# Kernel tuning notes

Hardware: AMD Instinct MI355X
Metric: run time of the kernel (lower is better)

## Reference

```python
import jax, jax.numpy as jnp
import numpy as np

B, C_LOCAL, C_GUIDE, C2, H, W = 16, 256, 256, 256, 64, 64
MID = C2 // 2          # mlp hidden channels
CQ = C_LOCAL // 4      # offset_gen hidden channels (also = groups)
EPS = 1e-5             # BatchNorm eps (inference mode)


def _conv(x, w, pad=0, groups=1, b=None):
    out = jax.lax.conv_general_dilated(
        x, w, window_strides=(1, 1), padding=((pad, pad), (pad, pad)),
        dimension_numbers=('NCHW', 'OIHW', 'NCHW'), feature_group_count=groups)
    if b is not None:
        out = out + b[None, :, None, None]
    return out


def _bn(x, g, b, m, v):
    scale = g / jnp.sqrt(v + EPS)
    return x * scale[None, :, None, None] + (b - m * scale)[None, :, None, None]


def _grid_sample(img, grid):
    # img: [C,H,W]; grid: [H,W,2] with (x,y) in [-1,1]; bilinear, zeros padding,
    # align_corners=False (pixel = ((g+1)*size - 1)/2)
    C, Hh, Ww = img.shape
    ix = (grid[..., 0] + 1.0) * (Ww * 0.5) - 0.5
    iy = (grid[..., 1] + 1.0) * (Hh * 0.5) - 0.5
    x0 = jnp.floor(ix); y0 = jnp.floor(iy)
    x1 = x0 + 1.0;      y1 = y0 + 1.0
    wx1 = ix - x0; wx0 = 1.0 - wx1
    wy1 = iy - y0; wy0 = 1.0 - wy1

    def gather(xi, yi):
        valid = (xi >= 0) & (xi < Ww) & (yi >= 0) & (yi < Hh)
        xc = jnp.clip(xi, 0, Ww - 1).astype(jnp.int32)
        yc = jnp.clip(yi, 0, Hh - 1).astype(jnp.int32)
        return img[:, yc, xc] * valid.astype(img.dtype)[None]  # [C,H,W]

    return (gather(x0, y0) * (wx0 * wy0)[None]
            + gather(x1, y0) * (wx1 * wy0)[None]
            + gather(x0, y1) * (wx0 * wy1)[None]
            + gather(x1, y1) * (wx1 * wy1)[None])


def setup_inputs() -> dict:
    key = jax.random.key(0)
    ks = jax.random.split(key, 20)
    w = lambda k, s: jax.random.normal(k, s, jnp.float32) * 0.05
    return {
        'x_local': jax.random.normal(ks[0], (B, C_LOCAL, H, W), jnp.float32),
        'x_guide': jax.random.normal(ks[1], (B, C_GUIDE, H, W), jnp.float32),
        'w_align': w(ks[2], (C2, C_GUIDE, 1, 1)),
        'bn1_g': 1.0 + 0.1 * jax.random.normal(ks[3], (C2,), jnp.float32),
        'bn1_b': 0.1 * jax.random.normal(ks[4], (C2,), jnp.float32),
        'bn1_m': 0.1 * jax.random.normal(ks[5], (C2,), jnp.float32),
        'bn1_v': 0.5 + jax.random.uniform(ks[6], (C2,), jnp.float32),
        'w_off1': w(ks[7], (CQ, 4, 3, 3)),   # grouped: in-ch per group = C_LOCAL/CQ = 4
        'w_off2': w(ks[8], (2, CQ, 1, 1)),
        'b_off2': 0.1 * jax.random.normal(ks[9], (2,), jnp.float32),
        'w_mlp1': w(ks[10], (MID, C_LOCAL, 1, 1)),
        'bn2_g': 1.0 + 0.1 * jax.random.normal(ks[11], (MID,), jnp.float32),
        'bn2_b': 0.1 * jax.random.normal(ks[12], (MID,), jnp.float32),
        'bn2_m': 0.1 * jax.random.normal(ks[13], (MID,), jnp.float32),
        'bn2_v': 0.5 + jax.random.uniform(ks[14], (MID,), jnp.float32),
        'w_mlp2': w(ks[15], (C2, MID, 1, 1)),
    }


def reference(x_local, x_guide, w_align, bn1_g, bn1_b, bn1_m, bn1_v,
              w_off1, w_off2, b_off2, w_mlp1, bn2_g, bn2_b, bn2_m, bn2_v,
              w_mlp2):
    # align(x_guide): 1x1 conv + BN
    g = _bn(_conv(x_guide, w_align), bn1_g, bn1_b, bn1_m, bn1_v)
    # offset_gen(x_local): grouped 3x3 conv -> SiLU -> 1x1 conv (bias) -> [B,2,H,W]
    off = _conv(x_local, w_off1, pad=1, groups=CQ)
    off = _conv(jax.nn.silu(off), w_off2, b=b_off2)
    # base grid in [-1,1], (x,y) last
    ys = jnp.linspace(-1.0, 1.0, H)
    xs = jnp.linspace(-1.0, 1.0, W)
    gy, gx = jnp.meshgrid(ys, xs, indexing='ij')
    base = jnp.stack((gx, gy), axis=-1)                      # [H,W,2]
    v_grid = base[None] + off.transpose(0, 2, 3, 1) * (2.0 / max(H, W))
    g_aligned = jax.vmap(_grid_sample)(g, v_grid)            # [B,C2,H,W]
    # mlp(x_local): 1x1 conv -> BN -> GELU(exact) -> 1x1 conv
    l = _conv(x_local, w_mlp1)
    l = jax.nn.gelu(_bn(l, bn2_g, bn2_b, bn2_m, bn2_v), approximate=False)
    l = _conv(l, w_mlp2)
    return jax.nn.silu(g_aligned + l)
```

## Files before the change

kernel.cpp:

```cpp
#include <hip/hip_runtime.h>

typedef unsigned short u16;
typedef unsigned int u32;
typedef __bf16 bf16x8 __attribute__((ext_vector_type(8)));
typedef float f32x4 __attribute__((ext_vector_type(4)));
typedef u16 u16x4 __attribute__((ext_vector_type(4)));
typedef u16 u16x8 __attribute__((ext_vector_type(8)));

#define EPS 1e-5f

__device__ __forceinline__ u16 f2bf(float f) {
  unsigned u = __builtin_bit_cast(unsigned, f);
  u += 0x7FFFu + ((u >> 16) & 1u);
  return (u16)(u >> 16);
}
__device__ __forceinline__ float bf2f(u16 h) {
  unsigned u = ((unsigned)h) << 16;
  return __builtin_bit_cast(float, u);
}

__global__ void prep_weights(
    const float* __restrict__ wa, const float* __restrict__ g1, const float* __restrict__ b1,
    const float* __restrict__ m1, const float* __restrict__ v1,
    const float* __restrict__ w1, const float* __restrict__ g2, const float* __restrict__ b2,
    const float* __restrict__ m2, const float* __restrict__ v2,
    const float* __restrict__ w2,
    u16* __restrict__ Acat, u16* __restrict__ w1_o,
    float* __restrict__ bias1, float* __restrict__ bias2) {
  int c = blockIdx.x, k = threadIdx.x;
  float s1 = g1[c] / sqrtf(v1[c] + EPS);
  if (k < 256) Acat[c * 384 + k] = f2bf(wa[c * 256 + k] * s1);
  else         Acat[c * 384 + k] = f2bf(w2[c * 128 + (k - 256)]);
  if (c < 128) {
    float s2 = g2[c] / sqrtf(v2[c] + EPS);
    if (k < 256) w1_o[c * 256 + k] = f2bf(w1[c * 256 + k] * s2);
    if (k == 256) bias2[c] = b2[c] - m2[c] * s2;
  }
  if (k == 0) bias1[c] = b1[c] - m1[c] * s1;
}

__global__ __launch_bounds__(256) void gconv_kernel(
    const float* __restrict__ xl, const float* __restrict__ w1,
    u16* __restrict__ sbuf) {
  __shared__ float tile[4][18][68];
  const int tid = threadIdx.x;
  const int band = blockIdx.x;
  const int q = blockIdx.y;
  const int b = blockIdx.z;
  const float* xb = xl + ((size_t)b * 256 + 4 * q) * 4096;

  if (tid < 72) {
    int ci0 = tid / 18, r0_ = tid - ci0 * 18;
    float* rowp = &tile[ci0][r0_][0];
    rowp[0] = 0.f; rowp[65] = 0.f; rowp[66] = 0.f; rowp[67] = 0.f;
  }

  const int ci = tid >> 6, col = tid & 63;
  const int gy0 = band * 16 - 1;
  const float* cp = xb + (size_t)ci * 4096 + col;
  float v[18];
#pragma unroll
  for (int r = 0; r < 18; ++r) {
    int gy = gy0 + r;
    int gyc = min(max(gy, 0), 63);
    float raw = cp[gyc * 64];
    v[r] = ((unsigned)gy < 64u) ? raw : 0.f;
  }
#pragma unroll
  for (int r = 0; r < 18; ++r) tile[ci][r][col + 1] = v[r];

  float wq[36];
#pragma unroll
  for (int i = 0; i < 36; ++i) wq[i] = w1[q * 36 + i];
  __syncthreads();

  const int qx = tid & 15, ry = tid >> 4;
  float a0 = 0.f, a1 = 0.f, a2 = 0.f, a3 = 0.f;
#pragma unroll
  for (int ci2 = 0; ci2 < 4; ++ci2) {
#pragma unroll
    for (int dy = 0; dy < 3; ++dy) {
      const float* rowp = &tile[ci2][ry + dy][qx * 4];
      f32x4 m = *(const f32x4*)rowp;
      float2 e = *(const float2*)(rowp + 4);
      float w0 = wq[ci2 * 9 + dy * 3 + 0];
      float w1_ = wq[ci2 * 9 + dy * 3 + 1];
      float w2_ = wq[ci2 * 9 + dy * 3 + 2];
      a0 += w0 * m[0] + w1_ * m[1] + w2_ * m[2];
      a1 += w0 * m[1] + w1_ * m[2] + w2_ * m[3];
      a2 += w0 * m[2] + w1_ * m[3] + w2_ * e.x;
      a3 += w0 * m[3] + w1_ * e.x  + w2_ * e.y;
    }
  }
  u16x4 o;
  o[0] = f2bf(a0 / (1.f + __expf(-a0)));
  o[1] = f2bf(a1 / (1.f + __expf(-a1)));
  o[2] = f2bf(a2 / (1.f + __expf(-a2)));
  o[3] = f2bf(a3 / (1.f + __expf(-a3)));
  u16* sp = sbuf + ((size_t)(b * 64 + q)) * 4096 + (band * 16 + ry) * 64 + qx * 4;
  *(u16x4*)sp = o;
}

__global__ __launch_bounds__(256) void coords_kernel(
    const u16* __restrict__ sbuf, const float* __restrict__ w2,
    const float* __restrict__ b2, float* __restrict__ coords,
    float* __restrict__ wsum) {
  __shared__ float sw2[128];
  const int tid = threadIdx.x;
  if (tid < 128) sw2[tid] = w2[tid];
  __syncthreads();
  const int b = blockIdx.y;
  const int p = blockIdx.x * 256 + tid;
  const u16* sp = sbuf + (size_t)b * 64 * 4096 + p;
  float ax = 0.f, ay = 0.f;
#pragma unroll 8
  for (int q = 0; q < 64; ++q) {
    float v = bf2f(sp[(size_t)q * 4096]);
    ax += sw2[q] * v;
    ay += sw2[64 + q] * v;
  }
  int y = p >> 6, x = p & 63;
  float ix = (64.f / 63.f) * (float)x + ax + b2[0] - 0.5f;
  float iy = (64.f / 63.f) * (float)y + ay + b2[1] - 0.5f;
  ((float2*)coords)[(size_t)b * 4096 + p] = make_float2(ix, iy);
  float x0f = floorf(ix), y0f = floorf(iy);
  int x0 = (int)x0f, y0 = (int)y0f;
  float wx1 = ix - x0f, wx0 = 1.f - wx1;
  float wy1 = iy - y0f, wy0 = 1.f - wy1;
  bool vx0 = (unsigned)x0 < 64u, vx1 = (unsigned)(x0 + 1) < 64u;
  bool vy0 = (unsigned)y0 < 64u, vy1 = (unsigned)(y0 + 1) < 64u;
  float s = (vx0 && vy0 ? wx0 * wy0 : 0.f) + (vx1 && vy0 ? wx1 * wy0 : 0.f) +
            (vx0 && vy1 ? wx0 * wy1 : 0.f) + (vx1 && vy1 ? wx1 * wy1 : 0.f);
  wsum[(size_t)b * 4096 + p] = s;
}

__global__ __launch_bounds__(256, 1) void sampler_kernel(
    const float* __restrict__ xg, const float* __restrict__ coords,
    u16* __restrict__ xh) {
  __shared__ u16 t[64 * 72];
  const int wg = blockIdx.x;
  const int id = (wg & 7) * 512 + (wg >> 3);
  const int kq = id >> 10;
  const int b = (id >> 6) & 15, row = id & 63;
  const int tid = threadIdx.x;
  const int px = tid & 63, ko = tid >> 6;
  const int p = row * 64 + px;
  float2 cd = ((const float2*)coords)[(size_t)b * 4096 + p];
  float ix = cd.x, iy = cd.y;
  float x0f = floorf(ix), y0f = floorf(iy);
  int x0 = (int)x0f, y0 = (int)y0f;
  float wx1 = ix - x0f, wx0 = 1.f - wx1;
  float wy1 = iy - y0f, wy0 = 1.f - wy1;
  bool vx0 = (unsigned)x0 < 64u, vx1 = (unsigned)(x0 + 1) < 64u;
  bool vy0 = (unsigned)y0 < 64u, vy1 = (unsigned)(y0 + 1) < 64u;
  int x0c = min(max(x0, 0), 63), x1c = min(max(x0 + 1, 0), 63);
  int y0c = min(max(y0, 0), 63), y1c = min(max(y0 + 1, 0), 63);
  float w00 = (vx0 && vy0) ? wx0 * wy0 : 0.f;
  float w10 = (vx1 && vy0) ? wx1 * wy0 : 0.f;
  float w01 = (vx0 && vy1) ? wx0 * wy1 : 0.f;
  float w11 = (vx1 && vy1) ? wx1 * wy1 : 0.f;
  const int i00 = y0c * 64 + x0c, i10 = y0c * 64 + x1c;
  const int i01 = y1c * 64 + x0c, i11 = y1c * 64 + x1c;
  const float* bb = xg + ((size_t)b * 256 + kq * 64 + ko * 16) * 4096;

  float v00[16], v10[16], v01[16], v11[16];
#pragma unroll
  for (int kk = 0; kk < 16; ++kk) {
    const float* bp = bb + (size_t)kk * 4096;
    v00[kk] = bp[i00];
    v10[kk] = bp[i10];
    v01[kk] = bp[i01];
    v11[kk] = bp[i11];
  }
  u16 o[16];
#pragma unroll
  for (int kk = 0; kk < 16; ++kk) {
    float v = w00 * v00[kk] + w10 * v10[kk] + w01 * v01[kk] + w11 * v11[kk];
    o[kk] = f2bf(v);
  }
  *(u16x8*)&t[px * 72 + ko * 16] = *(u16x8*)&o[0];
  *(u16x8*)&t[px * 72 + ko * 16 + 8] = *(u16x8*)&o[8];
  __syncthreads();
  const int seg = tid & 7, pxa = tid >> 3;
  u16* base = xh + ((size_t)b * 4096 + row * 64) * 384 + kq * 64 + seg * 8;
#pragma unroll
  for (int h = 0; h < 2; ++h) {
    int pp = pxa + h * 32;
    *(u16x8*)(base + (size_t)pp * 384) = *(const u16x8*)&t[pp * 72 + seg * 8];
  }
}

__global__ __launch_bounds__(256, 2) void gemm_h(
    const u16* __restrict__ A, const float* __restrict__ Bsrc,
    u16* __restrict__ xh, const float* __restrict__ bias) {
  __shared__ u16 Al[128][40];
  __shared__ u16 Bl[128][40];
  const int tid = threadIdx.x;
  const int b = blockIdx.y;
  const int n0 = blockIdx.x * 128;
  const int wave = tid >> 6, lane = tid & 63;
  const int wr = wave >> 1, wc = wave & 1;
  const int lr = lane & 15, kg = lane >> 4;
  f32x4 acc[4][4] = {};
  const float* Bf = Bsrc + (size_t)b * 256 * 4096;

  for (int kt = 0; kt < 8; ++kt) {
    {
      int m = tid >> 1, pos = (tid & 1) * 16;
      u16x8 v0 = *(const u16x8*)(A + (size_t)m * 256 + kt * 32 + pos);
      u16x8 v1 = *(const u16x8*)(A + (size_t)m * 256 + kt * 32 + pos + 8);
      *(u16x8*)&Al[m][pos] = v0;
      *(u16x8*)&Al[m][pos + 8] = v1;
    }
    {
      int nq = tid & 31, kq = tid >> 5;
      int kb = kt * 32 + kq * 4;
      int nb = n0 + nq * 4;
      f32x4 r[4];
#pragma unroll
      for (int i = 0; i < 4; ++i)
        r[i] = *(const f32x4*)(Bf + (size_t)(kb + i) * 4096 + nb);
#pragma unroll
      for (int j = 0; j < 4; ++j) {
        u16x4 w = {f2bf(r[0][j]), f2bf(r[1][j]), f2bf(r[2][j]), f2bf(r[3][j])};
        *(u16x4*)&Bl[nq * 4 + j][kq * 4] = w;
      }
    }
    __syncthreads();
    bf16x8 af[4], bfr[4];
#pragma unroll
    for (int i = 0; i < 4; ++i) {
      af[i] = *(const bf16x8*)&Al[wr * 64 + i * 16 + lr][kg * 8];
      bfr[i] = *(const bf16x8*)&Bl[wc * 64 + i * 16 + lr][kg * 8];
    }
#pragma unroll
    for (int i = 0; i < 4; ++i)
#pragma unroll
      for (int j = 0; j < 4; ++j)
        acc[i][j] = __builtin_amdgcn_mfma_f32_16x16x32_bf16(af[i], bfr[j], acc[i][j], 0, 0, 0);
    __syncthreads();
  }
  u16* O = xh + (size_t)b * 4096 * 384 + 256;
#pragma unroll
  for (int i = 0; i < 4; ++i) {
    int rb = wr * 64 + i * 16 + kg * 4;
    f32x4 b4 = *(const f32x4*)(bias + rb);
#pragma unroll
    for (int j = 0; j < 4; ++j) {
      int col = n0 + wc * 64 + j * 16 + lr;
      u16x4 w;
#pragma unroll
      for (int e = 0; e < 4; ++e) {
        float v = acc[i][j][e] + b4[e];
        v = 0.5f * v * (1.f + erff(v * 0.70710678118f));
        w[e] = f2bf(v);
      }
      *(u16x4*)(O + (size_t)col * 384 + rb) = w;
    }
  }
}

__global__ __launch_bounds__(256) void gemm_final(
    const u16* __restrict__ A,
    const u16* __restrict__ xh,
    const float* __restrict__ bias1, const float* __restrict__ wsum,
    float* __restrict__ out) {
  __shared__ u16 Al[128][40];
  __shared__ u16 Bl[128][40];
  const int tid = threadIdx.x;
  const int wg = blockIdx.y * 64 + blockIdx.x;
  const int nmb = (wg & 7) * 128 + (wg >> 3);
  const int m = nmb & 1;
  const int n0 = ((nmb >> 1) & 31) * 128;
  const int b = nmb >> 6;
  const int wave = tid >> 6, lane = tid & 63;
  const int wr = wave >> 1, wc = wave & 1;
  const int lr = lane & 15, kg = lane >> 4;
  f32x4 acc[4][4] = {};
  const u16* Ab = A + (size_t)m * 128 * 384;
  const u16* Bb = xh + ((size_t)b * 4096 + n0) * 384;

  for (int kt = 0; kt < 12; ++kt) {
#pragma unroll
    for (int c = 0; c < 2; ++c) {
      int ch = tid + c * 256;
      int r = ch >> 2, pos = (ch & 3) * 8;
      *(u16x8*)&Al[r][pos] = *(const u16x8*)(Ab + (size_t)r * 384 + kt * 32 + pos);
      *(u16x8*)&Bl[r][pos] = *(const u16x8*)(Bb + (size_t)r * 384 + kt * 32 + pos);
    }
    __syncthreads();
    bf16x8 af[4], bfr[4];
#pragma unroll
    for (int i = 0; i < 4; ++i) {
      af[i] = *(const bf16x8*)&Al[wr * 64 + i * 16 + lr][kg * 8];
      bfr[i] = *(const bf16x8*)&Bl[wc * 64 + i * 16 + lr][kg * 8];
    }
#pragma unroll
    for (int i = 0; i < 4; ++i)
#pragma unroll
      for (int j = 0; j < 4; ++j)
        acc[i][j] = __builtin_amdgcn_mfma_f32_16x16x32_bf16(af[i], bfr[j], acc[i][j], 0, 0, 0);
    __syncthreads();
  }

  float* Ob = out + (size_t)b * 256 * 4096;
#pragma unroll
  for (int j = 0; j < 4; ++j) {
    int col = n0 + wc * 64 + j * 16 + lr;
    float ws = wsum[(size_t)b * 4096 + col];
#pragma unroll
    for (int i = 0; i < 4; ++i) {
      int rb = m * 128 + wr * 64 + i * 16 + kg * 4;
      f32x4 b4 = *(const f32x4*)(bias1 + rb);
#pragma unroll
      for (int e = 0; e < 4; ++e) {
        float v = acc[i][j][e] + b4[e] * ws;
        Ob[(size_t)(rb + e) * 4096 + col] = v / (1.f + __expf(-v));
      }
    }
  }
}

extern "C" void kernel_launch(void* const* d_in, const int* in_sizes, int n_in,
                              void* d_out, int out_size, void* d_ws, size_t ws_size,
                              hipStream_t stream) {
  const float* x_local = (const float*)d_in[0];
  const float* x_guide = (const float*)d_in[1];
  const float* w_align = (const float*)d_in[2];
  const float* bn1_g = (const float*)d_in[3];
  const float* bn1_b = (const float*)d_in[4];
  const float* bn1_m = (const float*)d_in[5];
  const float* bn1_v = (const float*)d_in[6];
  const float* w_off1 = (const float*)d_in[7];
  const float* w_off2 = (const float*)d_in[8];
  const float* b_off2 = (const float*)d_in[9];
  const float* w_mlp1 = (const float*)d_in[10];
  const float* bn2_g = (const float*)d_in[11];
  const float* bn2_b = (const float*)d_in[12];
  const float* bn2_m = (const float*)d_in[13];
  const float* bn2_v = (const float*)d_in[14];
  const float* w_mlp2 = (const float*)d_in[15];

  char* ws = (char*)d_ws;
  u16* Acat = (u16*)(ws + 0);
  u16* w1_bf = (u16*)(ws + 196608);
  float* bias1 = (float*)(ws + 262144);
  float* bias2 = (float*)(ws + 263168);
  float* wsum = (float*)(ws + 263680);
  float* coords = (float*)(ws + 525824);
  u16* xh = (u16*)(ws + 1050112);
  u16* sbuf = xh;

  prep_weights<<<256, 384, 0, stream>>>(
      w_align, bn1_g, bn1_b, bn1_m, bn1_v,
      w_mlp1, bn2_g, bn2_b, bn2_m, bn2_v, w_mlp2,
      Acat, w1_bf, bias1, bias2);

  gconv_kernel<<<dim3(4, 64, 16), 256, 0, stream>>>(x_local, w_off1, sbuf);

  coords_kernel<<<dim3(16, 16), 256, 0, stream>>>(sbuf, w_off2, b_off2, coords, wsum);

  sampler_kernel<<<4096, 256, 0, stream>>>(x_guide, coords, xh);

  gemm_h<<<dim3(32, 16), 256, 0, stream>>>(w1_bf, x_local, xh, bias2);

  gemm_final<<<dim3(64, 16), 256, 0, stream>>>(Acat, xh, bias1, wsum, (float*)d_out);
}
```

Measured before the change: 111.8 us.

## Double-buffer LDS tiles and register-prefetch next K-slice in both GEMMs

Both GEMM kernels now keep two LDS buffers and prefetch the next K-slice from global memory into registers while the current slice runs through MFMA. This removes the second __syncthreads per iteration and overlaps global load latency with compute. In exchange it doubles LDS use per block and raises register pressure, which could lower occupancy, especially in gemm_h with launch_bounds(256,2).

New measurement: 110.9 us. No clear change (-0.8%).

```diff
diff --git a/kernel.cpp b/kernel.cpp
--- a/kernel.cpp
+++ b/kernel.cpp
@@ -193,8 +193,8 @@
 __global__ __launch_bounds__(256, 2) void gemm_h(
     const u16* __restrict__ A, const float* __restrict__ Bsrc,
     u16* __restrict__ xh, const float* __restrict__ bias) {
-  __shared__ u16 Al[128][40];
-  __shared__ u16 Bl[128][40];
+  __shared__ u16 Al[2][128][40];
+  __shared__ u16 Bl[2][128][40];
   const int tid = threadIdx.x;
   const int b = blockIdx.y;
   const int n0 = blockIdx.x * 128;
@@ -204,41 +204,49 @@
   f32x4 acc[4][4] = {};
   const float* Bf = Bsrc + (size_t)b * 256 * 4096;
 
+  const int am = tid >> 1, apos = (tid & 1) * 16;
+  const int nq = tid & 31, kq = tid >> 5;
+  const int nb = n0 + nq * 4;
+
+  u16x8 qa0, qa1;
+  f32x4 qb[4];
+  {
+    qa0 = *(const u16x8*)(A + (size_t)am * 256 + 0 + apos);
+    qa1 = *(const u16x8*)(A + (size_t)am * 256 + 0 + apos + 8);
+#pragma unroll
+    for (int i = 0; i < 4; ++i)
+      qb[i] = *(const f32x4*)(Bf + (size_t)(kq * 4 + i) * 4096 + nb);
+  }
+  int cur = 0;
   for (int kt = 0; kt < 8; ++kt) {
-    {
-      int m = tid >> 1, pos = (tid & 1) * 16;
-      u16x8 v0 = *(const u16x8*)(A + (size_t)m * 256 + kt * 32 + pos);
-      u16x8 v1 = *(const u16x8*)(A + (size_t)m * 256 + kt * 32 + pos + 8);
-      *(u16x8*)&Al[m][pos] = v0;
-      *(u16x8*)&Al[m][pos + 8] = v1;
-    }
-    {
-      int nq = tid & 31, kq = tid >> 5;
-      int kb = kt * 32 + kq * 4;
-      int nb = n0 + nq * 4;
-      f32x4 r[4];
+    *(u16x8*)&Al[cur][am][apos] = qa0;
+    *(u16x8*)&Al[cur][am][apos + 8] = qa1;
+#pragma unroll
+    for (int j = 0; j < 4; ++j) {
+      u16x4 w = {f2bf(qb[0][j]), f2bf(qb[1][j]), f2bf(qb[2][j]), f2bf(qb[3][j])};
+      *(u16x4*)&Bl[cur][nq * 4 + j][kq * 4] = w;
+    }
+    if (kt < 7) {
+      int k1 = (kt + 1) * 32;
+      qa0 = *(const u16x8*)(A + (size_t)am * 256 + k1 + apos);
+      qa1 = *(const u16x8*)(A + (size_t)am * 256 + k1 + apos + 8);
 #pragma unroll
       for (int i = 0; i < 4; ++i)
-        r[i] = *(const f32x4*)(Bf + (size_t)(kb + i) * 4096 + nb);
-#pragma unroll
-      for (int j = 0; j < 4; ++j) {
-        u16x4 w = {f2bf(r[0][j]), f2bf(r[1][j]), f2bf(r[2][j]), f2bf(r[3][j])};
-        *(u16x4*)&Bl[nq * 4 + j][kq * 4] = w;
-      }
+        qb[i] = *(const f32x4*)(Bf + (size_t)(k1 + kq * 4 + i) * 4096 + nb);
     }
     __syncthreads();
     bf16x8 af[4], bfr[4];
 #pragma unroll
     for (int i = 0; i < 4; ++i) {
-      af[i] = *(const bf16x8*)&Al[wr * 64 + i * 16 + lr][kg * 8];
-      bfr[i] = *(const bf16x8*)&Bl[wc * 64 + i * 16 + lr][kg * 8];
+      af[i] = *(const bf16x8*)&Al[cur][wr * 64 + i * 16 + lr][kg * 8];
+      bfr[i] = *(const bf16x8*)&Bl[cur][wc * 64 + i * 16 + lr][kg * 8];
     }
 #pragma unroll
     for (int i = 0; i < 4; ++i)
 #pragma unroll
       for (int j = 0; j < 4; ++j)
         acc[i][j] = __builtin_amdgcn_mfma_f32_16x16x32_bf16(af[i], bfr[j], acc[i][j], 0, 0, 0);
-    __syncthreads();
+    cur ^= 1;
   }
   u16* O = xh + (size_t)b * 4096 * 384 + 256;
 #pragma unroll
@@ -265,8 +273,8 @@
     const u16* __restrict__ xh,
     const float* __restrict__ bias1, const float* __restrict__ wsum,
     float* __restrict__ out) {
-  __shared__ u16 Al[128][40];
-  __shared__ u16 Bl[128][40];
+  __shared__ u16 Al[2][128][40];
+  __shared__ u16 Bl[2][128][40];
   const int tid = threadIdx.x;
   const int wg = blockIdx.y * 64 + blockIdx.x;
   const int nmb = (wg & 7) * 128 + (wg >> 3);
@@ -280,27 +288,42 @@
   const u16* Ab = A + (size_t)m * 128 * 384;
   const u16* Bb = xh + ((size_t)b * 4096 + n0) * 384;
 
+  const int r0 = tid >> 2, pos0 = (tid & 3) * 8;
+  const int r1 = (tid + 256) >> 2, pos1 = pos0;
+
+  u16x8 pa0, pa1, pb0, pb1;
+  {
+    pa0 = *(const u16x8*)(Ab + (size_t)r0 * 384 + 0 + pos0);
+    pb0 = *(const u16x8*)(Bb + (size_t)r0 * 384 + 0 + pos0);
+    pa1 = *(const u16x8*)(Ab + (size_t)r1 * 384 + 0 + pos1);
+    pb1 = *(const u16x8*)(Bb + (size_t)r1 * 384 + 0 + pos1);
+  }
+  int cur = 0;
   for (int kt = 0; kt < 12; ++kt) {
-#pragma unroll
-    for (int c = 0; c < 2; ++c) {
-      int ch = tid + c * 256;
-      int r = ch >> 2, pos = (ch & 3) * 8;
-      *(u16x8*)&Al[r][pos] = *(const u16x8*)(Ab + (size_t)r * 384 + kt * 32 + pos);
-      *(u16x8*)&Bl[r][pos] = *(const u16x8*)(Bb + (size_t)r * 384 + kt * 32 + pos);
+    *(u16x8*)&Al[cur][r0][pos0] = pa0;
+    *(u16x8*)&Bl[cur][r0][pos0] = pb0;
+    *(u16x8*)&Al[cur][r1][pos1] = pa1;
+    *(u16x8*)&Bl[cur][r1][pos1] = pb1;
+    if (kt < 11) {
+      int k1 = (kt + 1) * 32;
+      pa0 = *(const u16x8*)(Ab + (size_t)r0 * 384 + k1 + pos0);
+      pb0 = *(const u16x8*)(Bb + (size_t)r0 * 384 + k1 + pos0);
+      pa1 = *(const u16x8*)(Ab + (size_t)r1 * 384 + k1 + pos1);
+      pb1 = *(const u16x8*)(Bb + (size_t)r1 * 384 + k1 + pos1);
     }
     __syncthreads();
     bf16x8 af[4], bfr[4];
 #pragma unroll
     for (int i = 0; i < 4; ++i) {
-      af[i] = *(const bf16x8*)&Al[wr * 64 + i * 16 + lr][kg * 8];
-      bfr[i] = *(const bf16x8*)&Bl[wc * 64 + i * 16 + lr][kg * 8];
+      af[i] = *(const bf16x8*)&Al[cur][wr * 64 + i * 16 + lr][kg * 8];
+      bfr[i] = *(const bf16x8*)&Bl[cur][wc * 64 + i * 16 + lr][kg * 8];
     }
 #pragma unroll
     for (int i = 0; i < 4; ++i)
 #pragma unroll
       for (int j = 0; j < 4; ++j)
         acc[i][j] = __builtin_amdgcn_mfma_f32_16x16x32_bf16(af[i], bfr[j], acc[i][j], 0, 0, 0);
-    __syncthreads();
+    cur ^= 1;
   }
 
   float* Ob = out + (size_t)b * 256 * 4096;
```
